# Kernel tuning notes

Hardware: AMD Instinct MI355X
Metric: run time of the kernel (lower is better)

Reference implementation:

```python
import jax, jax.numpy as jnp
import numpy as np

IMAGE_SIZE = 256
PSIZE = 6
STRIDE = 2
WINDOW = IMAGE_SIZE + 1 - PSIZE  # 251
CUR = np.arange(0, WINDOW, STRIDE)
if CUR[-1] != WINDOW - 1:
    CUR = np.concatenate([CUR, np.array([WINDOW - 1])])
NPOS = len(CUR)  # 126 strided window positions per axis
BATCH = 128


def setup_inputs() -> dict:
    key = jax.random.key(0)
    x = jax.random.normal(key, (BATCH, 1, IMAGE_SIZE, IMAGE_SIZE), dtype=jnp.float32)
    return {"x": x}


def reference(x):
    # Equivalent to patch_tf.forward(to_patch): for each strided window position
    # (r, c) in CUR x CUR and each in-patch offset (i, j) in [0, PSIZE)^2,
    # output[b, r*NPOS + c, i*PSIZE + j] = x[b, 0, r + i, c + j].
    cur = jnp.asarray(CUR, dtype=jnp.int32)          # [NPOS]
    off = jnp.arange(PSIZE, dtype=jnp.int32)         # [PSIZE]
    row_idx = cur[:, None] + off[None, :]            # [NPOS, PSIZE]
    col_idx = cur[:, None] + off[None, :]            # [NPOS, PSIZE]
    img = x[:, 0]                                    # [B, H, W]
    # Advanced-index gather -> [B, NPOS, NPOS, PSIZE, PSIZE]
    patches = img[:, row_idx[:, None, :, None], col_idx[None, :, None, :]]
    return patches.reshape(x.shape[0], NPOS * NPOS, PSIZE * PSIZE)
```

## Files before the change

### kernel.cpp

```cpp
#include <hip/hip_runtime.h>


#define IMG 256
#define PSZ 6
#define NPOS 126
#define BATCHN 128
#define LDSW 257
#define VECS_PER_BAND 1134

__global__ __launch_bounds__(256) void image2patch_kernel(
    const float* __restrict__ x, float* __restrict__ out) {
  __shared__ float tile[PSZ * LDSW];

  const int blk = blockIdx.x;
  const int b = blk / NPOS;
  const int i = blk - b * NPOS;
  const int t = threadIdx.x;

  const float* src = x + (size_t)b * (IMG * IMG) + (size_t)(2 * i) * IMG;
  for (int idx = t; idx < PSZ * (IMG / 4); idx += 256) {
    const int row  = idx >> 6;
    const int col4 = idx & 63;
    float4 v = reinterpret_cast<const float4*>(src + row * IMG)[col4];
    float* d = &tile[row * LDSW + col4 * 4];
    d[0] = v.x; d[1] = v.y; d[2] = v.z; d[3] = v.w;
  }
  __syncthreads();

  float4* outp = reinterpret_cast<float4*>(
      out + ((size_t)b * (NPOS * NPOS) + (size_t)i * NPOS) * (PSZ * PSZ));
  for (int q = t; q < VECS_PER_BAND; q += 256) {
    const int f  = q * 4;
    const int j  = f / 36;
    const int k0 = f - j * 36;
    const int jj = 2 * j;
    float4 v;
    { const int k = k0;     const int r = k / PSZ, c = k - PSZ * r; v.x = tile[r * LDSW + jj + c]; }
    { const int k = k0 + 1; const int r = k / PSZ, c = k - PSZ * r; v.y = tile[r * LDSW + jj + c]; }
    { const int k = k0 + 2; const int r = k / PSZ, c = k - PSZ * r; v.z = tile[r * LDSW + jj + c]; }
    { const int k = k0 + 3; const int r = k / PSZ, c = k - PSZ * r; v.w = tile[r * LDSW + jj + c]; }
    outp[q] = v;
  }
}

extern "C" void kernel_launch(void* const* d_in, const int* in_sizes, int n_in,
                              void* d_out, int out_size, void* d_ws, size_t ws_size,
                              hipStream_t stream) {
  const float* x = (const float*)d_in[0];
  float* out = (float*)d_out;
  image2patch_kernel<<<BATCHN * NPOS, 256, 0, stream>>>(x, out);
}
```

Before: 313.6 us.

## Precompute LDS gather addresses per thread, remap blocks across XCDs, repad LDS

Each thread now handles a fixed in-patch offset pattern, with 252 threads covering 28 patches per pass. Its four LDS addresses are computed once and advanced by a constant stride, which removes the per-element divisions in the output loop. Block indices are remapped so that consecutive bands for the same image land on the same XCD, which should improve L2 reuse of the overlapping input rows. The LDS row pitch is changed to 267 and the load loop is reordered row-fastest to alter the bank conflict pattern. This leaves 4 threads idle and puts a half-active tail on the last iteration.

Measured after the change: 313.3 us. Within noise of the previous version (-0.1%).

```diff
diff --git a/kernel.cpp b/kernel.cpp
--- a/kernel.cpp
+++ b/kernel.cpp
@@ -5,41 +5,65 @@
 #define PSZ 6
 #define NPOS 126
 #define BATCHN 128
-#define LDSW 257
-#define VECS_PER_BAND 1134
+#define LDSW 267
+#define NV 1134
+#define NXCD 8
 
 __global__ __launch_bounds__(256) void image2patch_kernel(
     const float* __restrict__ x, float* __restrict__ out) {
   __shared__ float tile[PSZ * LDSW];
 
-  const int blk = blockIdx.x;
+  const int cpx = (BATCHN * NPOS) / NXCD;
+  const int raw = blockIdx.x;
+  const int blk = (raw % NXCD) * cpx + raw / NXCD;
+
   const int b = blk / NPOS;
   const int i = blk - b * NPOS;
   const int t = threadIdx.x;
 
   const float* src = x + (size_t)b * (IMG * IMG) + (size_t)(2 * i) * IMG;
   for (int idx = t; idx < PSZ * (IMG / 4); idx += 256) {
-    const int row  = idx >> 6;
-    const int col4 = idx & 63;
+    const int col4 = idx / PSZ;
+    const int row  = idx - col4 * PSZ;
     float4 v = reinterpret_cast<const float4*>(src + row * IMG)[col4];
     float* d = &tile[row * LDSW + col4 * 4];
     d[0] = v.x; d[1] = v.y; d[2] = v.z; d[3] = v.w;
   }
   __syncthreads();
 
-  float4* outp = reinterpret_cast<float4*>(
-      out + ((size_t)b * (NPOS * NPOS) + (size_t)i * NPOS) * (PSZ * PSZ));
-  for (int q = t; q < VECS_PER_BAND; q += 256) {
-    const int f  = q * 4;
-    const int j  = f / 36;
-    const int k0 = f - j * 36;
-    const int jj = 2 * j;
-    float4 v;
-    { const int k = k0;     const int r = k / PSZ, c = k - PSZ * r; v.x = tile[r * LDSW + jj + c]; }
-    { const int k = k0 + 1; const int r = k / PSZ, c = k - PSZ * r; v.y = tile[r * LDSW + jj + c]; }
-    { const int k = k0 + 2; const int r = k / PSZ, c = k - PSZ * r; v.z = tile[r * LDSW + jj + c]; }
-    { const int k = k0 + 3; const int r = k / PSZ, c = k - PSZ * r; v.w = tile[r * LDSW + jj + c]; }
-    outp[q] = v;
+  if (t < 252) {
+    const int tj = t / 9;
+    const int m  = t - 9 * tj;
+    const int k0 = 4 * m;
+    int a0, a1, a2, a3;
+    {
+      const int k = k0;     const int r = k / PSZ, c = k - PSZ * r; a0 = r * LDSW + 2 * tj + c;
+    }
+    {
+      const int k = k0 + 1; const int r = k / PSZ, c = k - PSZ * r; a1 = r * LDSW + 2 * tj + c;
+    }
+    {
+      const int k = k0 + 2; const int r = k / PSZ, c = k - PSZ * r; a2 = r * LDSW + 2 * tj + c;
+    }
+    {
+      const int k = k0 + 3; const int r = k / PSZ, c = k - PSZ * r; a3 = r * LDSW + 2 * tj + c;
+    }
+    float4* outp = reinterpret_cast<float4*>(
+        out + ((size_t)b * (NPOS * NPOS) + (size_t)i * NPOS) * (PSZ * PSZ));
+    int q = t;
+#pragma unroll
+    for (int it = 0; it < 4; ++it) {
+      float4 v;
+      v.x = tile[a0]; v.y = tile[a1]; v.z = tile[a2]; v.w = tile[a3];
+      outp[q] = v;
+      a0 += 56; a1 += 56; a2 += 56; a3 += 56;
+      q += 252;
+    }
+    if (t < 126) {
+      float4 v;
+      v.x = tile[a0]; v.y = tile[a1]; v.z = tile[a2]; v.w = tile[a3];
+      outp[q] = v;
+    }
   }
 }
 
```
